# Optimization experiments

Hardware: AMD Instinct MI355X
Metric: run time of the kernel (lower is better)

Reference implementation:

```python
import jax, jax.numpy as jnp
import numpy as np

B, H, W, D = 8, 128, 128, 256
NHEAD, DK = 8, 32
WS = 8
NH, NW = H // WS, W // WS
SHIFT = WS // 2
SCALE = 1.0 / np.sqrt(DK)
WSQ = WS * WS


def _region_labels(h, w, ws, shift):
    lab = np.zeros((h, w), np.int32)
    cnt = 0
    for hs in (slice(0, h - ws), slice(h - ws, h - shift), slice(h - shift, h)):
        for vs in (slice(0, w - ws), slice(w - ws, w - shift), slice(w - shift, w)):
            lab[hs, vs] = cnt
            cnt += 1
    return np.roll(lab, (-shift, -shift), axis=(0, 1))


def _window_labels(lab, ws, nh, nw):
    return lab.reshape(nh, ws, nw, ws).transpose(0, 2, 1, 3).reshape(nh, nw, ws * ws)


# static Swin attention mask: (nh, nw, WSQ, WSQ) bool, True = masked
_lq = _window_labels(_region_labels(H, W, WS, SHIFT), WS, NH, NW)
_lk = _window_labels(_region_labels(H, W, WS, SHIFT), WS, NH, NW)
MASK = jnp.asarray(_lq[..., :, None] != _lk[..., None, :])

# static relative position index: (WSQ, WSQ) into (2*WS-1)^2 table
_coords = np.stack(np.meshgrid(np.arange(WS), np.arange(WS), indexing='ij'), -1).reshape(-1, 2)
_rel = _coords[:, None, :] - _coords[None, :, :] + (WS - 1)  # in [0, 2*WS-2]
REL_INDEX = jnp.asarray(_rel[..., 0] * (2 * WS - 1) + _rel[..., 1])


def _cyclic_shift(t, s):
    # t: (B, nhead, H, W, d)
    return jnp.roll(t, (-s, -s), axis=(2, 3))


def _partition(t):
    # (B, nhead, H, W, d) -> (B, nhead, NH, NW, WSQ, d)
    b, nh_, _, _, d = t.shape
    t = t.reshape(b, nh_, NH, WS, NW, WS, d)
    return t.transpose(0, 1, 2, 4, 3, 5, 6).reshape(b, nh_, NH, NW, WSQ, d)


def _merge(t):
    # (B, nhead, NH, NW, WSQ, d) -> (B, nhead, H, W, d)
    b, nh_, _, _, _, d = t.shape
    t = t.reshape(b, nh_, NH, NW, WS, WS, d).transpose(0, 1, 2, 4, 3, 5, 6)
    return t.reshape(b, nh_, NH * WS, NW * WS, d)


def setup_inputs() -> dict:
    key = jax.random.key(0)
    ks = jax.random.split(key, 6)
    return {
        'x': jax.random.normal(ks[0], (B, H, W, D), jnp.float32),
        'z': jax.random.normal(ks[1], (B, H, W, D), jnp.float32),
        'Wq': jax.random.normal(ks[2], (D, D), jnp.float32) * 0.02,
        'bq': jnp.zeros((D,), jnp.float32),
        'Wkv': jax.random.normal(ks[3], (D, 2 * D), jnp.float32) * 0.02,
        'bkv': jnp.zeros((2 * D,), jnp.float32),
        'Wo': jax.random.normal(ks[4], (D, D), jnp.float32) * 0.02,
        'bo': jnp.zeros((D,), jnp.float32),
        'rel_table': jax.random.normal(ks[5], ((2 * WS - 1) ** 2, NHEAD), jnp.float32) * 0.02,
    }


def reference(x, z, Wq, bq, Wkv, bkv, Wo, bo, rel_table):
    b = x.shape[0]
    q = (x @ Wq + bq).reshape(b, H, W, NHEAD, DK).transpose(0, 3, 1, 2, 4)
    kv = (z @ Wkv + bkv).reshape(b, H, W, 2, NHEAD, DK).transpose(3, 0, 4, 1, 2, 5)
    k, v = kv[0], kv[1]

    q = _partition(_cyclic_shift(q, SHIFT))
    k = _partition(_cyclic_shift(k, SHIFT))
    v = _partition(_cyclic_shift(v, SHIFT))

    # scores: (B, nhead, NH, NW, WSQ, WSQ)
    scores = jnp.einsum('bhijqd,bhijkd->bhijqk', q, k) * SCALE
    pe = rel_table[REL_INDEX]                       # (WSQ, WSQ, nhead)
    scores = scores + pe.transpose(2, 0, 1)[None, :, None, None]
    scores = jnp.where(MASK, jnp.float32(-1e9), scores)
    attn = jax.nn.softmax(scores, axis=-1)

    out = jnp.einsum('bhijqk,bhijkd->bhijqd', attn, v)
    out = _cyclic_shift(_merge(out), -SHIFT)        # (B, nhead, H, W, DK)
    out = out.transpose(0, 2, 3, 1, 4).reshape(b, H, W, D)
    return out @ Wo + bo
```

## Files before the change

### kernel.cpp

```cpp
#include <hip/hip_runtime.h>
#include <hip/hip_bf16.h>


typedef __bf16  bf16x8 __attribute__((ext_vector_type(8)));
typedef short   short8 __attribute__((ext_vector_type(8)));
typedef float   f32x4  __attribute__((ext_vector_type(4)));

#define SCALE_F 0.17677669529663687f

#define ZS   16896
#define WB   33792
#define WSZ  5120
#define LDS_TOT 74752

__device__ __forceinline__ short f2bs(float f){
    __hip_bfloat16 h = __float2bfloat16(f);
    return __builtin_bit_cast(short, h);
}
__device__ __forceinline__ short8 cvt8(float4 a, float4 b){
    short8 t;
    t[0]=f2bs(a.x); t[1]=f2bs(a.y); t[2]=f2bs(a.z); t[3]=f2bs(a.w);
    t[4]=f2bs(b.x); t[5]=f2bs(b.y); t[6]=f2bs(b.z); t[7]=f2bs(b.w);
    return t;
}
__device__ __forceinline__ int strip3(int r, int c){
    if (c == 0) return 0;
    if (c == 1) return (r < 4) ? 0 : 1;
    return (r < 4) ? 2 : 0;
}

__global__ __launch_bounds__(256) void prep_k(const float* __restrict__ Wq,
                                              const float* __restrict__ Wkv,
                                              const float* __restrict__ Wo,
                                              const float* __restrict__ rel,
                                              short* __restrict__ Wqt,
                                              short* __restrict__ Wkvt,
                                              short* __restrict__ Wot,
                                              float* __restrict__ ADD){
    int i = blockIdx.x * 256 + threadIdx.x;
    if (i < 65536){
        int n = i >> 8, k = i & 255;
        Wqt[i] = f2bs(Wq[k * 256 + n]);
    } else if (i < 196608){
        int j = i - 65536;
        int n = j >> 8, k = j & 255;
        Wkvt[j] = f2bs(Wkv[k * 512 + n]);
    } else if (i < 262144){
        int j = i - 196608;
        int n = j >> 8, k = j & 255;
        Wot[j] = f2bs(Wo[k * 256 + n]);
    } else {
        int j = i - 262144;
        int k = j & 63, q = (j >> 6) & 63, head = (j >> 12) & 7, cls = j >> 15;
        int wiC = cls / 3, wjC = cls - wiC * 3;
        int qr = q >> 3, qc = q & 7, kr = k >> 3, kc = k & 7;
        int lq = strip3(qr, wiC) * 3 + strip3(qc, wjC);
        int lk = strip3(kr, wiC) * 3 + strip3(kc, wjC);
        float pe = rel[((qr - kr + 7) * 15 + (qc - kc + 7)) * 8 + head];
        ADD[j] = (lq != lk) ? -1e9f : pe;
    }
}

__global__ __launch_bounds__(512, 2) void fused_k(
    const float* __restrict__ x, const float* __restrict__ z,
    const short* __restrict__ Wqt, const short* __restrict__ Wkvt,
    const short* __restrict__ Wot,
    const float* __restrict__ bq, const float* __restrict__ bkv,
    const float* __restrict__ bo,
    const float* __restrict__ ADD, float* __restrict__ out){
    __shared__ __align__(16) short lds[LDS_TOT];
    const int tid = threadIdx.x, w = tid >> 6, lane = tid & 63;
    const int l15 = lane & 15, g = lane >> 4;
    const int bx = blockIdx.x;
    const int wj = bx & 15, wi = (bx >> 4) & 15, b = bx >> 8;
    const int wiC = (wi > 13) ? wi - 13 : 0;
    const int wjC = (wj > 13) ? wj - 13 : 0;
    const f32x4 zero = {0.f,0.f,0.f,0.f};

#pragma unroll
    for (int i=0;i<4;++i){
        const int u = tid + i*512;
        const int p = u >> 5, c8 = u & 31;
        const int pr = ((wi << 3) + (p >> 3) + 4) & 127;
        const int pc = ((wj << 3) + (p & 7) + 4) & 127;
        const size_t gidx = ((((((size_t)b << 7) | pr) << 7) | pc) << 8) + c8*8;
        const float4* xp = reinterpret_cast<const float4*>(x + gidx);
        float4 a0 = xp[0], a1 = xp[1];
        *reinterpret_cast<short8*>(lds + p*264 + c8*8) = cvt8(a0, a1);
        const float4* zp = reinterpret_cast<const float4*>(z + gidx);
        float4 b0 = zp[0], b1 = zp[1];
        *reinterpret_cast<short8*>(lds + ZS + p*264 + c8*8) = cvt8(b0, b1);
    }
    __syncthreads();

    short* R  = lds + WB + w*WSZ;
    short* VL = lds + w*2048;
    const int c0 = w*32;

    {
        bf16x8 wf[8][2];
#pragma unroll
        for (int kt=0;kt<8;++kt)
#pragma unroll
            for (int nj=0;nj<2;++nj)
                wf[kt][nj] = *reinterpret_cast<const bf16x8*>(Wqt + (size_t)(c0 + nj*16 + l15)*256 + kt*32 + g*8);
        f32x4 acc[4][2];
#pragma unroll
        for (int mi=0;mi<4;++mi){ acc[mi][0]=zero; acc[mi][1]=zero; }
#pragma unroll
        for (int kt=0;kt<8;++kt){
            bf16x8 af[4];
#pragma unroll
            for (int mi=0;mi<4;++mi)
                af[mi] = *reinterpret_cast<const bf16x8*>(lds + (mi*16 + l15)*264 + kt*32 + g*8);
#pragma unroll
            for (int mi=0;mi<4;++mi)
#pragma unroll
                for (int nj=0;nj<2;++nj)
                    acc[mi][nj] = __builtin_amdgcn_mfma_f32_16x16x32_bf16(af[mi], wf[kt][nj], acc[mi][nj], 0,0,0);
        }
#pragma unroll
        for (int nj=0;nj<2;++nj){
            float bv = bq[c0 + nj*16 + l15];
#pragma unroll
            for (int mi=0;mi<4;++mi)
#pragma unroll
                for (int r=0;r<4;++r)
                    R[(mi*16 + g*4 + r)*40 + nj*16 + l15] = f2bs(acc[mi][nj][r] + bv);
        }
    }
    {
        bf16x8 wf[8][2];
#pragma unroll
        for (int kt=0;kt<8;++kt)
#pragma unroll
            for (int nj=0;nj<2;++nj)
                wf[kt][nj] = *reinterpret_cast<const bf16x8*>(Wkvt + (size_t)(c0 + nj*16 + l15)*256 + kt*32 + g*8);
        f32x4 acc[4][2];
#pragma unroll
        for (int mi=0;mi<4;++mi){ acc[mi][0]=zero; acc[mi][1]=zero; }
#pragma unroll
        for (int kt=0;kt<8;++kt){
            bf16x8 af[4];
#pragma unroll
            for (int mi=0;mi<4;++mi)
                af[mi] = *reinterpret_cast<const bf16x8*>(lds + ZS + (mi*16 + l15)*264 + kt*32 + g*8);
#pragma unroll
            for (int mi=0;mi<4;++mi)
#pragma unroll
                for (int nj=0;nj<2;++nj)
                    acc[mi][nj] = __builtin_amdgcn_mfma_f32_16x16x32_bf16(af[mi], wf[kt][nj], acc[mi][nj], 0,0,0);
        }
#pragma unroll
        for (int nj=0;nj<2;++nj){
            float bv = bkv[c0 + nj*16 + l15];
#pragma unroll
            for (int mi=0;mi<4;++mi)
#pragma unroll
                for (int r=0;r<4;++r)
                    R[2560 + (mi*16 + g*4 + r)*40 + nj*16 + l15] = f2bs(acc[mi][nj][r] + bv);
        }
    }
    __syncthreads();
    {
        bf16x8 wf[8][2];
#pragma unroll
        for (int kt=0;kt<8;++kt)
#pragma unroll
            for (int nj=0;nj<2;++nj)
                wf[kt][nj] = *reinterpret_cast<const bf16x8*>(Wkvt + (size_t)(256 + c0 + nj*16 + l15)*256 + kt*32 + g*8);
        f32x4 acc[4][2];
#pragma unroll
        for (int mi=0;mi<4;++mi){ acc[mi][0]=zero; acc[mi][1]=zero; }
#pragma unroll
        for (int kt=0;kt<8;++kt){
            bf16x8 af[4];
#pragma unroll
            for (int mi=0;mi<4;++mi)
                af[mi] = *reinterpret_cast<const bf16x8*>(lds + ZS + (mi*16 + l15)*264 + kt*32 + g*8);
#pragma unroll
            for (int mi=0;mi<4;++mi)
#pragma unroll
                for (int nj=0;nj<2;++nj)
                    acc[mi][nj] = __builtin_amdgcn_mfma_f32_16x16x32_bf16(af[mi], wf[kt][nj], acc[mi][nj], 0,0,0);
        }
        const int sw = (l15 & 7) << 3;
#pragma unroll
        for (int nj=0;nj<2;++nj){
            float bv = bkv[256 + c0 + nj*16 + l15];
            const int colb = (nj*16 + l15) * 64;
#pragma unroll
            for (int mi=0;mi<4;++mi)
#pragma unroll
                for (int r=0;r<4;++r)
                    VL[(colb + mi*16 + g*4 + r) ^ sw] = f2bs(acc[mi][nj][r] + bv);
        }
    }

    bf16x8 aq[4], bk[4];
#pragma unroll
    for (int mi=0;mi<4;++mi) aq[mi] = *reinterpret_cast<const bf16x8*>(R + (mi*16 + l15)*40 + g*8);
#pragma unroll
    for (int ni=0;ni<4;++ni) bk[ni] = *reinterpret_cast<const bf16x8*>(R + 2560 + (ni*16 + l15)*40 + g*8);
    f32x4 s[4][4];
#pragma unroll
    for (int mi=0;mi<4;++mi)
#pragma unroll
        for (int ni=0;ni<4;++ni)
            s[mi][ni] = __builtin_amdgcn_mfma_f32_16x16x32_bf16(aq[mi], bk[ni], zero, 0,0,0);

    const float* addb = ADD + (size_t)(((wiC*3 + wjC)*8 + w) << 12);
    float rs[4][4];
#pragma unroll
    for (int mi=0;mi<4;++mi){
        const int qbase = mi*16 + g*4;
#pragma unroll
        for (int ni=0;ni<4;++ni){
            const int k = ni*16 + l15;
#pragma unroll
            for (int r=0;r<4;++r)
                s[mi][ni][r] = fmaf(s[mi][ni][r], SCALE_F, addb[((qbase + r) << 6) + k]);
        }
#pragma unroll
        for (int r=0;r<4;++r){
            float m = fmaxf(fmaxf(s[mi][0][r], s[mi][1][r]), fmaxf(s[mi][2][r], s[mi][3][r]));
            m = fmaxf(m, __shfl_xor(m, 1));
            m = fmaxf(m, __shfl_xor(m, 2));
            m = fmaxf(m, __shfl_xor(m, 4));
            m = fmaxf(m, __shfl_xor(m, 8));
            float sum = 0.f;
#pragma unroll
            for (int ni=0;ni<4;++ni){
                float p = __expf(s[mi][ni][r] - m);
                s[mi][ni][r] = p;
                sum += p;
            }
            sum += __shfl_xor(sum, 1);
            sum += __shfl_xor(sum, 2);
            sum += __shfl_xor(sum, 4);
            sum += __shfl_xor(sum, 8);
            rs[mi][r] = 1.f / sum;
            const int q = qbase + r;
#pragma unroll
            for (int ni=0;ni<4;++ni)
                R[q*72 + ni*16 + l15] = f2bs(s[mi][ni][r]);
        }
    }

    f32x4 o[4][2];
#pragma unroll
    for (int mi=0;mi<4;++mi){ o[mi][0]=zero; o[mi][1]=zero; }
    {
        const int sw = (l15 & 7) << 3;
#pragma unroll
        for (int ks=0;ks<2;++ks){
            bf16x8 pa[4], vb[2];
#pragma unroll
            for (int mi=0;mi<4;++mi)
                pa[mi] = *reinterpret_cast<const bf16x8*>(R + (mi*16 + l15)*72 + ks*32 + g*8);
#pragma unroll
            for (int nj=0;nj<2;++nj)
                vb[nj] = *reinterpret_cast<const bf16x8*>(VL + (((nj*16 + l15)*64 + ks*32 + g*8) ^ sw));
#pragma unroll
            for (int mi=0;mi<4;++mi)
#pragma unroll
                for (int nj=0;nj<2;++nj)
                    o[mi][nj] = __builtin_amdgcn_mfma_f32_16x16x32_bf16(pa[mi], vb[nj], o[mi][nj], 0,0,0);
        }
    }

#pragma unroll
    for (int mi=0;mi<4;++mi)
#pragma unroll
        for (int nj=0;nj<2;++nj)
#pragma unroll
            for (int r=0;r<4;++r)
                R[(mi*16 + g*4 + r)*40 + nj*16 + l15] = f2bs(o[mi][nj][r] * rs[mi][r]);
    __syncthreads();

    {
        bf16x8 wf[8][2];
#pragma unroll
        for (int kt=0;kt<8;++kt)
#pragma unroll
            for (int nj=0;nj<2;++nj)
                wf[kt][nj] = *reinterpret_cast<const bf16x8*>(Wot + (size_t)(c0 + nj*16 + l15)*256 + kt*32 + g*8);
        f32x4 acc[4][2];
#pragma unroll
        for (int mi=0;mi<4;++mi){ acc[mi][0]=zero; acc[mi][1]=zero; }
#pragma unroll
        for (int kt=0;kt<8;++kt){
            const short* areg = lds + WB + kt*WSZ;
            bf16x8 af[4];
#pragma unroll
            for (int mi=0;mi<4;++mi)
                af[mi] = *reinterpret_cast<const bf16x8*>(areg + (mi*16 + l15)*40 + g*8);
#pragma unroll
            for (int mi=0;mi<4;++mi)
#pragma unroll
                for (int nj=0;nj<2;++nj)
                    acc[mi][nj] = __builtin_amdgcn_mfma_f32_16x16x32_bf16(af[mi], wf[kt][nj], acc[mi][nj], 0,0,0);
        }
#pragma unroll
        for (int nj=0;nj<2;++nj){
            const int col = c0 + nj*16 + l15;
            const float bv = bo[col];
#pragma unroll
            for (int mi=0;mi<4;++mi)
#pragma unroll
                for (int r=0;r<4;++r){
                    const int p = mi*16 + g*4 + r;
                    const int pr = ((wi << 3) + (p >> 3) + 4) & 127;
                    const int pc = ((wj << 3) + (p & 7) + 4) & 127;
                    const size_t gp = ((((size_t)b << 7) | pr) << 7) | pc;
                    out[gp * 256 + col] = acc[mi][nj][r] + bv;
                }
        }
    }
}

extern "C" void kernel_launch(void* const* d_in, const int* in_sizes, int n_in,
                              void* d_out, int out_size, void* d_ws, size_t ws_size,
                              hipStream_t stream) {
    const float* x    = (const float*)d_in[0];
    const float* z    = (const float*)d_in[1];
    const float* Wq   = (const float*)d_in[2];
    const float* bq   = (const float*)d_in[3];
    const float* Wkv  = (const float*)d_in[4];
    const float* bkv  = (const float*)d_in[5];
    const float* Wo   = (const float*)d_in[6];
    const float* bo   = (const float*)d_in[7];
    const float* rel  = (const float*)d_in[8];

    char* ws = (char*)d_ws;
    short* Wqt  = (short*)(ws);
    short* Wkvt = (short*)(ws + 131072);
    short* Wot  = (short*)(ws + 393216);
    float* ADD  = (float*)(ws + 524288);

    prep_k<<<2176, 256, 0, stream>>>(Wq, Wkv, Wo, rel, Wqt, Wkvt, Wot, ADD);
    fused_k<<<2048, 512, 0, stream>>>(x, z, Wqt, Wkvt, Wot, bq, bkv, bo, ADD, (float*)d_out);
}
```

Measured before the change: 252.1 us.

## Split each head's window rows across two waves with 1024-thread blocks

The fused kernel now launches 1024 threads per block. Each of the eight heads is handled by two waves, and each wave processes 32 of the 64 window rows in the projections, scores, softmax, PV and output projection. This doubles resident waves per CU, since LDS already limits the kernel to one block per CU, and should give more latency hiding. In exchange it adds extra block-wide barriers to protect the shared R buffer, duplicates the weight-fragment loads per wave pair, and the (1024,4) launch bound may force a tight register budget and spilling.

```diff
diff --git a/kernel.cpp b/kernel.cpp
--- a/kernel.cpp
+++ b/kernel.cpp
@@ -61,7 +61,7 @@
     }
 }
 
-__global__ __launch_bounds__(512, 2) void fused_k(
+__global__ __launch_bounds__(1024, 4) void fused_k(
     const float* __restrict__ x, const float* __restrict__ z,
     const short* __restrict__ Wqt, const short* __restrict__ Wkvt,
     const short* __restrict__ Wot,
@@ -71,6 +71,7 @@
     __shared__ __align__(16) short lds[LDS_TOT];
     const int tid = threadIdx.x, w = tid >> 6, lane = tid & 63;
     const int l15 = lane & 15, g = lane >> 4;
+    const int h = w >> 1, m = w & 1, r0 = m * 32;
     const int bx = blockIdx.x;
     const int wj = bx & 15, wi = (bx >> 4) & 15, b = bx >> 8;
     const int wiC = (wi > 13) ? wi - 13 : 0;
@@ -78,8 +79,8 @@
     const f32x4 zero = {0.f,0.f,0.f,0.f};
 
 #pragma unroll
-    for (int i=0;i<4;++i){
-        const int u = tid + i*512;
+    for (int i=0;i<2;++i){
+        const int u = tid + i*1024;
         const int p = u >> 5, c8 = u & 31;
         const int pr = ((wi << 3) + (p >> 3) + 4) & 127;
         const int pc = ((wj << 3) + (p & 7) + 4) & 127;
@@ -93,9 +94,9 @@
     }
     __syncthreads();
 
-    short* R  = lds + WB + w*WSZ;
-    short* VL = lds + w*2048;
-    const int c0 = w*32;
+    short* R  = lds + WB + h*WSZ;
+    short* VL = lds + h*2048;
+    const int c0 = h*32;
 
     {
         bf16x8 wf[8][2];
@@ -104,17 +105,17 @@
 #pragma unroll
             for (int nj=0;nj<2;++nj)
                 wf[kt][nj] = *reinterpret_cast<const bf16x8*>(Wqt + (size_t)(c0 + nj*16 + l15)*256 + kt*32 + g*8);
-        f32x4 acc[4][2];
-#pragma unroll
-        for (int mi=0;mi<4;++mi){ acc[mi][0]=zero; acc[mi][1]=zero; }
+        f32x4 acc[2][2];
+#pragma unroll
+        for (int mi=0;mi<2;++mi){ acc[mi][0]=zero; acc[mi][1]=zero; }
 #pragma unroll
         for (int kt=0;kt<8;++kt){
-            bf16x8 af[4];
-#pragma unroll
-            for (int mi=0;mi<4;++mi)
-                af[mi] = *reinterpret_cast<const bf16x8*>(lds + (mi*16 + l15)*264 + kt*32 + g*8);
-#pragma unroll
-            for (int mi=0;mi<4;++mi)
+            bf16x8 af[2];
+#pragma unroll
+            for (int mi=0;mi<2;++mi)
+                af[mi] = *reinterpret_cast<const bf16x8*>(lds + (r0 + mi*16 + l15)*264 + kt*32 + g*8);
+#pragma unroll
+            for (int mi=0;mi<2;++mi)
 #pragma unroll
                 for (int nj=0;nj<2;++nj)
                     acc[mi][nj] = __builtin_amdgcn_mfma_f32_16x16x32_bf16(af[mi], wf[kt][nj], acc[mi][nj], 0,0,0);
@@ -123,10 +124,10 @@
         for (int nj=0;nj<2;++nj){
             float bv = bq[c0 + nj*16 + l15];
 #pragma unroll
-            for (int mi=0;mi<4;++mi)
+            for (int mi=0;mi<2;++mi)
 #pragma unroll
                 for (int r=0;r<4;++r)
-                    R[(mi*16 + g*4 + r)*40 + nj*16 + l15] = f2bs(acc[mi][nj][r] + bv);
+                    R[(r0 + mi*16 + g*4 + r)*40 + nj*16 + l15] = f2bs(acc[mi][nj][r] + bv);
         }
     }
     {
@@ -136,17 +137,17 @@
 #pragma unroll
             for (int nj=0;nj<2;++nj)
                 wf[kt][nj] = *reinterpret_cast<const bf16x8*>(Wkvt + (size_t)(c0 + nj*16 + l15)*256 + kt*32 + g*8);
-        f32x4 acc[4][2];
-#pragma unroll
-        for (int mi=0;mi<4;++mi){ acc[mi][0]=zero; acc[mi][1]=zero; }
+        f32x4 acc[2][2];
+#pragma unroll
+        for (int mi=0;mi<2;++mi){ acc[mi][0]=zero; acc[mi][1]=zero; }
 #pragma unroll
         for (int kt=0;kt<8;++kt){
-            bf16x8 af[4];
-#pragma unroll
-            for (int mi=0;mi<4;++mi)
-                af[mi] = *reinterpret_cast<const bf16x8*>(lds + ZS + (mi*16 + l15)*264 + kt*32 + g*8);
-#pragma unroll
-            for (int mi=0;mi<4;++mi)
+            bf16x8 af[2];
+#pragma unroll
+            for (int mi=0;mi<2;++mi)
+                af[mi] = *reinterpret_cast<const bf16x8*>(lds + ZS + (r0 + mi*16 + l15)*264 + kt*32 + g*8);
+#pragma unroll
+            for (int mi=0;mi<2;++mi)
 #pragma unroll
                 for (int nj=0;nj<2;++nj)
                     acc[mi][nj] = __builtin_amdgcn_mfma_f32_16x16x32_bf16(af[mi], wf[kt][nj], acc[mi][nj], 0,0,0);
@@ -155,13 +156,14 @@
         for (int nj=0;nj<2;++nj){
             float bv = bkv[c0 + nj*16 + l15];
 #pragma unroll
-            for (int mi=0;mi<4;++mi)
+            for (int mi=0;mi<2;++mi)
 #pragma unroll
                 for (int r=0;r<4;++r)
-                    R[2560 + (mi*16 + g*4 + r)*40 + nj*16 + l15] = f2bs(acc[mi][nj][r] + bv);
-        }
-    }
-    __syncthreads();
+                    R[2560 + (r0 + mi*16 + g*4 + r)*40 + nj*16 + l15] = f2bs(acc[mi][nj][r] + bv);
+        }
+    }
+    __syncthreads();
+
     {
         bf16x8 wf[8][2];
 #pragma unroll
@@ -169,17 +171,17 @@
 #pragma unroll
             for (int nj=0;nj<2;++nj)
                 wf[kt][nj] = *reinterpret_cast<const bf16x8*>(Wkvt + (size_t)(256 + c0 + nj*16 + l15)*256 + kt*32 + g*8);
-        f32x4 acc[4][2];
-#pragma unroll
-        for (int mi=0;mi<4;++mi){ acc[mi][0]=zero; acc[mi][1]=zero; }
+        f32x4 acc[2][2];
+#pragma unroll
+        for (int mi=0;mi<2;++mi){ acc[mi][0]=zero; acc[mi][1]=zero; }
 #pragma unroll
         for (int kt=0;kt<8;++kt){
-            bf16x8 af[4];
-#pragma unroll
-            for (int mi=0;mi<4;++mi)
-                af[mi] = *reinterpret_cast<const bf16x8*>(lds + ZS + (mi*16 + l15)*264 + kt*32 + g*8);
-#pragma unroll
-            for (int mi=0;mi<4;++mi)
+            bf16x8 af[2];
+#pragma unroll
+            for (int mi=0;mi<2;++mi)
+                af[mi] = *reinterpret_cast<const bf16x8*>(lds + ZS + (r0 + mi*16 + l15)*264 + kt*32 + g*8);
+#pragma unroll
+            for (int mi=0;mi<2;++mi)
 #pragma unroll
                 for (int nj=0;nj<2;++nj)
                     acc[mi][nj] = __builtin_amdgcn_mfma_f32_16x16x32_bf16(af[mi], wf[kt][nj], acc[mi][nj], 0,0,0);
@@ -190,30 +192,31 @@
             float bv = bkv[256 + c0 + nj*16 + l15];
             const int colb = (nj*16 + l15) * 64;
 #pragma unroll
-            for (int mi=0;mi<4;++mi)
+            for (int mi=0;mi<2;++mi)
 #pragma unroll
                 for (int r=0;r<4;++r)
-                    VL[(colb + mi*16 + g*4 + r) ^ sw] = f2bs(acc[mi][nj][r] + bv);
-        }
-    }
-
-    bf16x8 aq[4], bk[4];
-#pragma unroll
-    for (int mi=0;mi<4;++mi) aq[mi] = *reinterpret_cast<const bf16x8*>(R + (mi*16 + l15)*40 + g*8);
+                    VL[(colb + r0 + mi*16 + g*4 + r) ^ sw] = f2bs(acc[mi][nj][r] + bv);
+        }
+    }
+
+    bf16x8 aq[2], bk[4];
+#pragma unroll
+    for (int mi=0;mi<2;++mi) aq[mi] = *reinterpret_cast<const bf16x8*>(R + (r0 + mi*16 + l15)*40 + g*8);
 #pragma unroll
     for (int ni=0;ni<4;++ni) bk[ni] = *reinterpret_cast<const bf16x8*>(R + 2560 + (ni*16 + l15)*40 + g*8);
-    f32x4 s[4][4];
-#pragma unroll
-    for (int mi=0;mi<4;++mi)
+    f32x4 s[2][4];
+#pragma unroll
+    for (int mi=0;mi<2;++mi)
 #pragma unroll
         for (int ni=0;ni<4;++ni)
             s[mi][ni] = __builtin_amdgcn_mfma_f32_16x16x32_bf16(aq[mi], bk[ni], zero, 0,0,0);
-
-    const float* addb = ADD + (size_t)(((wiC*3 + wjC)*8 + w) << 12);
-    float rs[4][4];
-#pragma unroll
-    for (int mi=0;mi<4;++mi){
-        const int qbase = mi*16 + g*4;
+    __syncthreads();
+
+    const float* addb = ADD + (size_t)(((wiC*3 + wjC)*8 + h) << 12);
+    float rs[2][4];
+#pragma unroll
+    for (int mi=0;mi<2;++mi){
+        const int qbase = r0 + mi*16 + g*4;
 #pragma unroll
         for (int ni=0;ni<4;++ni){
             const int k = ni*16 + l15;
@@ -223,15 +226,15 @@
         }
 #pragma unroll
         for (int r=0;r<4;++r){
-            float m = fmaxf(fmaxf(s[mi][0][r], s[mi][1][r]), fmaxf(s[mi][2][r], s[mi][3][r]));
-            m = fmaxf(m, __shfl_xor(m, 1));
-            m = fmaxf(m, __shfl_xor(m, 2));
-            m = fmaxf(m, __shfl_xor(m, 4));
-            m = fmaxf(m, __shfl_xor(m, 8));
+            float mx = fmaxf(fmaxf(s[mi][0][r], s[mi][1][r]), fmaxf(s[mi][2][r], s[mi][3][r]));
+            mx = fmaxf(mx, __shfl_xor(mx, 1));
+            mx = fmaxf(mx, __shfl_xor(mx, 2));
+            mx = fmaxf(mx, __shfl_xor(mx, 4));
+            mx = fmaxf(mx, __shfl_xor(mx, 8));
             float sum = 0.f;
 #pragma unroll
             for (int ni=0;ni<4;++ni){
-                float p = __expf(s[mi][ni][r] - m);
+                float p = __expf(s[mi][ni][r] - mx);
                 s[mi][ni][r] = p;
                 sum += p;
             }
@@ -247,35 +250,36 @@
         }
     }
 
-    f32x4 o[4][2];
-#pragma unroll
-    for (int mi=0;mi<4;++mi){ o[mi][0]=zero; o[mi][1]=zero; }
+    f32x4 o[2][2];
+#pragma unroll
+    for (int mi=0;mi<2;++mi){ o[mi][0]=zero; o[mi][1]=zero; }
     {
         const int sw = (l15 & 7) << 3;
 #pragma unroll
         for (int ks=0;ks<2;++ks){
-            bf16x8 pa[4], vb[2];
-#pragma unroll
-            for (int mi=0;mi<4;++mi)
-                pa[mi] = *reinterpret_cast<const bf16x8*>(R + (mi*16 + l15)*72 + ks*32 + g*8);
+            bf16x8 pa[2], vb[2];
+#pragma unroll
+            for (int mi=0;mi<2;++mi)
+                pa[mi] = *reinterpret_cast<const bf16x8*>(R + (r0 + mi*16 + l15)*72 + ks*32 + g*8);
 #pragma unroll
             for (int nj=0;nj<2;++nj)
                 vb[nj] = *reinterpret_cast<const bf16x8*>(VL + (((nj*16 + l15)*64 + ks*32 + g*8) ^ sw));
 #pragma unroll
-            for (int mi=0;mi<4;++mi)
+            for (int mi=0;mi<2;++mi)
 #pragma unroll
                 for (int nj=0;nj<2;++nj)
                     o[mi][nj] = __builtin_amdgcn_mfma_f32_16x16x32_bf16(pa[mi], vb[nj], o[mi][nj], 0,0,0);
         }
     }
-
-#pragma unroll
-    for (int mi=0;mi<4;++mi)
+    __syncthreads();
+
+#pragma unroll
+    for (int mi=0;mi<2;++mi)
 #pragma unroll
         for (int nj=0;nj<2;++nj)
 #pragma unroll
             for (int r=0;r<4;++r)
-                R[(mi*16 + g*4 + r)*40 + nj*16 + l15] = f2bs(o[mi][nj][r] * rs[mi][r]);
+                R[(r0 + mi*16 + g*4 + r)*40 + nj*16 + l15] = f2bs(o[mi][nj][r] * rs[mi][r]);
     __syncthreads();
 
     {
@@ -285,18 +289,18 @@
 #pragma unroll
             for (int nj=0;nj<2;++nj)
                 wf[kt][nj] = *reinterpret_cast<const bf16x8*>(Wot + (size_t)(c0 + nj*16 + l15)*256 + kt*32 + g*8);
-        f32x4 acc[4][2];
-#pragma unroll
-        for (int mi=0;mi<4;++mi){ acc[mi][0]=zero; acc[mi][1]=zero; }
+        f32x4 acc[2][2];
+#pragma unroll
+        for (int mi=0;mi<2;++mi){ acc[mi][0]=zero; acc[mi][1]=zero; }
 #pragma unroll
         for (int kt=0;kt<8;++kt){
             const short* areg = lds + WB + kt*WSZ;
-            bf16x8 af[4];
-#pragma unroll
-            for (int mi=0;mi<4;++mi)
-                af[mi] = *reinterpret_cast<const bf16x8*>(areg + (mi*16 + l15)*40 + g*8);
-#pragma unroll
-            for (int mi=0;mi<4;++mi)
+            bf16x8 af[2];
+#pragma unroll
+            for (int mi=0;mi<2;++mi)
+                af[mi] = *reinterpret_cast<const bf16x8*>(areg + (r0 + mi*16 + l15)*40 + g*8);
+#pragma unroll
+            for (int mi=0;mi<2;++mi)
 #pragma unroll
                 for (int nj=0;nj<2;++nj)
                     acc[mi][nj] = __builtin_amdgcn_mfma_f32_16x16x32_bf16(af[mi], wf[kt][nj], acc[mi][nj], 0,0,0);
@@ -306,10 +310,10 @@
             const int col = c0 + nj*16 + l15;
             const float bv = bo[col];
 #pragma unroll
-            for (int mi=0;mi<4;++mi)
+            for (int mi=0;mi<2;++mi)
 #pragma unroll
                 for (int r=0;r<4;++r){
-                    const int p = mi*16 + g*4 + r;
+                    const int p = r0 + mi*16 + g*4 + r;
                     const int pr = ((wi << 3) + (p >> 3) + 4) & 127;
                     const int pc = ((wj << 3) + (p & 7) + 4) & 127;
                     const size_t gp = ((((size_t)b << 7) | pr) << 7) | pc;
@@ -339,5 +343,5 @@
     float* ADD  = (float*)(ws + 524288);
 
     prep_k<<<2176, 256, 0, stream>>>(Wq, Wkv, Wo, rel, Wqt, Wkvt, Wot, ADD);
-    fused_k<<<2048, 512, 0, stream>>>(x, z, Wqt, Wkvt, Wot, bq, bkv, bo, ADD, (float*)d_out);
-}
+    fused_k<<<2048, 1024, 0, stream>>>(x, z, Wqt, Wkvt, Wot, bq, bkv, bo, ADD, (float*)d_out);
+}
```

Result: slower. 350.0 us (+38.8%).

## Split fused window-attention kernel into QKV projection and attention+output kernels

Applied to the files above, without the earlier changes.

Breaks the single fused kernel into two. The first projects Q, K and V and writes them as bf16 to global workspace. The second, with 256 threads per block and one wave handling two heads, computes attention and the output projection. Weight fragments are now loaded once per k-step instead of being preloaded into registers, and both kernels use less LDS, aiming for lower register and LDS pressure and higher occupancy. In exchange, roughly 200 MB of extra global write-then-read traffic for Q/K/V is added, plus an extra launch.

```diff
diff --git a/kernel.cpp b/kernel.cpp
--- a/kernel.cpp
+++ b/kernel.cpp
@@ -4,14 +4,10 @@
 
 typedef __bf16  bf16x8 __attribute__((ext_vector_type(8)));
 typedef short   short8 __attribute__((ext_vector_type(8)));
+typedef short   short4v __attribute__((ext_vector_type(4)));
 typedef float   f32x4  __attribute__((ext_vector_type(4)));
 
 #define SCALE_F 0.17677669529663687f
-
-#define ZS   16896
-#define WB   33792
-#define WSZ  5120
-#define LDS_TOT 74752
 
 __device__ __forceinline__ short f2bs(float f){
     __hip_bfloat16 h = __float2bfloat16(f);
@@ -61,20 +57,16 @@
     }
 }
 
-__global__ __launch_bounds__(512, 2) void fused_k(
+__global__ __launch_bounds__(512, 2) void qkv_k(
     const float* __restrict__ x, const float* __restrict__ z,
     const short* __restrict__ Wqt, const short* __restrict__ Wkvt,
-    const short* __restrict__ Wot,
     const float* __restrict__ bq, const float* __restrict__ bkv,
-    const float* __restrict__ bo,
-    const float* __restrict__ ADD, float* __restrict__ out){
-    __shared__ __align__(16) short lds[LDS_TOT];
+    short* __restrict__ Qw, short* __restrict__ Kw, short* __restrict__ Vw){
+    __shared__ __align__(16) short lds[2 * 16896];
     const int tid = threadIdx.x, w = tid >> 6, lane = tid & 63;
     const int l15 = lane & 15, g = lane >> 4;
     const int bx = blockIdx.x;
     const int wj = bx & 15, wi = (bx >> 4) & 15, b = bx >> 8;
-    const int wiC = (wi > 13) ? wi - 13 : 0;
-    const int wjC = (wj > 13) ? wj - 13 : 0;
     const f32x4 zero = {0.f,0.f,0.f,0.f};
 
 #pragma unroll
@@ -89,27 +81,23 @@
         *reinterpret_cast<short8*>(lds + p*264 + c8*8) = cvt8(a0, a1);
         const float4* zp = reinterpret_cast<const float4*>(z + gidx);
         float4 b0 = zp[0], b1 = zp[1];
-        *reinterpret_cast<short8*>(lds + ZS + p*264 + c8*8) = cvt8(b0, b1);
+        *reinterpret_cast<short8*>(lds + 16896 + p*264 + c8*8) = cvt8(b0, b1);
     }
     __syncthreads();
 
-    short* R  = lds + WB + w*WSZ;
-    short* VL = lds + w*2048;
-    const int c0 = w*32;
+    const int c0 = w * 32;
+    const size_t base = ((((size_t)b*8 + w)*16 + wi)*16 + wj) * 2048;
 
     {
-        bf16x8 wf[8][2];
-#pragma unroll
-        for (int kt=0;kt<8;++kt)
-#pragma unroll
-            for (int nj=0;nj<2;++nj)
-                wf[kt][nj] = *reinterpret_cast<const bf16x8*>(Wqt + (size_t)(c0 + nj*16 + l15)*256 + kt*32 + g*8);
         f32x4 acc[4][2];
 #pragma unroll
         for (int mi=0;mi<4;++mi){ acc[mi][0]=zero; acc[mi][1]=zero; }
 #pragma unroll
         for (int kt=0;kt<8;++kt){
-            bf16x8 af[4];
+            bf16x8 af[4], wf[2];
+#pragma unroll
+            for (int nj=0;nj<2;++nj)
+                wf[nj] = *reinterpret_cast<const bf16x8*>(Wqt + (size_t)(c0 + nj*16 + l15)*256 + kt*32 + g*8);
 #pragma unroll
             for (int mi=0;mi<4;++mi)
                 af[mi] = *reinterpret_cast<const bf16x8*>(lds + (mi*16 + l15)*264 + kt*32 + g*8);
@@ -117,7 +105,7 @@
             for (int mi=0;mi<4;++mi)
 #pragma unroll
                 for (int nj=0;nj<2;++nj)
-                    acc[mi][nj] = __builtin_amdgcn_mfma_f32_16x16x32_bf16(af[mi], wf[kt][nj], acc[mi][nj], 0,0,0);
+                    acc[mi][nj] = __builtin_amdgcn_mfma_f32_16x16x32_bf16(af[mi], wf[nj], acc[mi][nj], 0,0,0);
         }
 #pragma unroll
         for (int nj=0;nj<2;++nj){
@@ -126,30 +114,27 @@
             for (int mi=0;mi<4;++mi)
 #pragma unroll
                 for (int r=0;r<4;++r)
-                    R[(mi*16 + g*4 + r)*40 + nj*16 + l15] = f2bs(acc[mi][nj][r] + bv);
+                    Qw[base + (size_t)(mi*16 + g*4 + r)*32 + nj*16 + l15] = f2bs(acc[mi][nj][r] + bv);
         }
     }
     {
-        bf16x8 wf[8][2];
-#pragma unroll
-        for (int kt=0;kt<8;++kt)
-#pragma unroll
-            for (int nj=0;nj<2;++nj)
-                wf[kt][nj] = *reinterpret_cast<const bf16x8*>(Wkvt + (size_t)(c0 + nj*16 + l15)*256 + kt*32 + g*8);
         f32x4 acc[4][2];
 #pragma unroll
         for (int mi=0;mi<4;++mi){ acc[mi][0]=zero; acc[mi][1]=zero; }
 #pragma unroll
         for (int kt=0;kt<8;++kt){
-            bf16x8 af[4];
-#pragma unroll
-            for (int mi=0;mi<4;++mi)
-                af[mi] = *reinterpret_cast<const bf16x8*>(lds + ZS + (mi*16 + l15)*264 + kt*32 + g*8);
+            bf16x8 af[4], wf[2];
+#pragma unroll
+            for (int nj=0;nj<2;++nj)
+                wf[nj] = *reinterpret_cast<const bf16x8*>(Wkvt + (size_t)(c0 + nj*16 + l15)*256 + kt*32 + g*8);
+#pragma unroll
+            for (int mi=0;mi<4;++mi)
+                af[mi] = *reinterpret_cast<const bf16x8*>(lds + 16896 + (mi*16 + l15)*264 + kt*32 + g*8);
 #pragma unroll
             for (int mi=0;mi<4;++mi)
 #pragma unroll
                 for (int nj=0;nj<2;++nj)
-                    acc[mi][nj] = __builtin_amdgcn_mfma_f32_16x16x32_bf16(af[mi], wf[kt][nj], acc[mi][nj], 0,0,0);
+                    acc[mi][nj] = __builtin_amdgcn_mfma_f32_16x16x32_bf16(af[mi], wf[nj], acc[mi][nj], 0,0,0);
         }
 #pragma unroll
         for (int nj=0;nj<2;++nj){
@@ -158,164 +143,178 @@
             for (int mi=0;mi<4;++mi)
 #pragma unroll
                 for (int r=0;r<4;++r)
-                    R[2560 + (mi*16 + g*4 + r)*40 + nj*16 + l15] = f2bs(acc[mi][nj][r] + bv);
-        }
-    }
-    __syncthreads();
+                    Kw[base + (size_t)(mi*16 + g*4 + r)*32 + nj*16 + l15] = f2bs(acc[mi][nj][r] + bv);
+        }
+    }
     {
-        bf16x8 wf[8][2];
-#pragma unroll
-        for (int kt=0;kt<8;++kt)
-#pragma unroll
-            for (int nj=0;nj<2;++nj)
-                wf[kt][nj] = *reinterpret_cast<const bf16x8*>(Wkvt + (size_t)(256 + c0 + nj*16 + l15)*256 + kt*32 + g*8);
         f32x4 acc[4][2];
 #pragma unroll
         for (int mi=0;mi<4;++mi){ acc[mi][0]=zero; acc[mi][1]=zero; }
 #pragma unroll
         for (int kt=0;kt<8;++kt){
-            bf16x8 af[4];
-#pragma unroll
-            for (int mi=0;mi<4;++mi)
-                af[mi] = *reinterpret_cast<const bf16x8*>(lds + ZS + (mi*16 + l15)*264 + kt*32 + g*8);
+            bf16x8 af[4], wf[2];
+#pragma unroll
+            for (int nj=0;nj<2;++nj)
+                wf[nj] = *reinterpret_cast<const bf16x8*>(Wkvt + (size_t)(256 + c0 + nj*16 + l15)*256 + kt*32 + g*8);
+#pragma unroll
+            for (int mi=0;mi<4;++mi)
+                af[mi] = *reinterpret_cast<const bf16x8*>(lds + 16896 + (mi*16 + l15)*264 + kt*32 + g*8);
 #pragma unroll
             for (int mi=0;mi<4;++mi)
 #pragma unroll
                 for (int nj=0;nj<2;++nj)
-                    acc[mi][nj] = __builtin_amdgcn_mfma_f32_16x16x32_bf16(af[mi], wf[kt][nj], acc[mi][nj], 0,0,0);
-        }
-        const int sw = (l15 & 7) << 3;
+                    acc[mi][nj] = __builtin_amdgcn_mfma_f32_16x16x32_bf16(af[mi], wf[nj], acc[mi][nj], 0,0,0);
+        }
 #pragma unroll
         for (int nj=0;nj<2;++nj){
             float bv = bkv[256 + c0 + nj*16 + l15];
-            const int colb = (nj*16 + l15) * 64;
-#pragma unroll
-            for (int mi=0;mi<4;++mi)
+            const int dk = nj*16 + l15;
+#pragma unroll
+            for (int mi=0;mi<4;++mi){
+                short4v t;
+#pragma unroll
+                for (int r=0;r<4;++r) t[r] = f2bs(acc[mi][nj][r] + bv);
+                *reinterpret_cast<short4v*>(Vw + base + (size_t)dk*64 + mi*16 + g*4) = t;
+            }
+        }
+    }
+}
+
+__global__ __launch_bounds__(256, 2) void attnO_k(
+    const short* __restrict__ Qw, const short* __restrict__ Kw,
+    const short* __restrict__ Vw, const short* __restrict__ Wot,
+    const float* __restrict__ bo, const float* __restrict__ ADD,
+    float* __restrict__ out){
+    __shared__ __align__(16) short lds[4*4608 + 16896];
+    const int tid = threadIdx.x, w = tid >> 6, lane = tid & 63;
+    const int l15 = lane & 15, g = lane >> 4;
+    const int bx = blockIdx.x;
+    const int wj = bx & 15, wi = (bx >> 4) & 15, b = bx >> 8;
+    const int wiC = (wi > 13) ? wi - 13 : 0;
+    const int wjC = (wj > 13) ? wj - 13 : 0;
+    short* P   = lds + w * 4608;
+    short* att = lds + 18432;
+    const f32x4 zero = {0.f,0.f,0.f,0.f};
+
+    for (int hh = 0; hh < 2; ++hh){
+        const int h = w + hh * 4;
+        const size_t base = ((((size_t)b*8 + h)*16 + wi)*16 + wj) * 2048;
+
+        bf16x8 aq[4], bk[4];
+#pragma unroll
+        for (int mi=0;mi<4;++mi)
+            aq[mi] = *reinterpret_cast<const bf16x8*>(Qw + base + (size_t)(mi*16 + l15)*32 + g*8);
+#pragma unroll
+        for (int ni=0;ni<4;++ni)
+            bk[ni] = *reinterpret_cast<const bf16x8*>(Kw + base + (size_t)(ni*16 + l15)*32 + g*8);
+        f32x4 s[4][4];
+#pragma unroll
+        for (int mi=0;mi<4;++mi)
+#pragma unroll
+            for (int ni=0;ni<4;++ni)
+                s[mi][ni] = __builtin_amdgcn_mfma_f32_16x16x32_bf16(aq[mi], bk[ni], zero, 0,0,0);
+
+        const float* addb = ADD + (size_t)(((wiC*3 + wjC)*8 + h) << 12);
+        float rs[4][4];
+#pragma unroll
+        for (int mi=0;mi<4;++mi){
+            const int qbase = mi*16 + g*4;
+#pragma unroll
+            for (int ni=0;ni<4;++ni){
+                const int k = ni*16 + l15;
 #pragma unroll
                 for (int r=0;r<4;++r)
-                    VL[(colb + mi*16 + g*4 + r) ^ sw] = f2bs(acc[mi][nj][r] + bv);
-        }
-    }
-
-    bf16x8 aq[4], bk[4];
-#pragma unroll
-    for (int mi=0;mi<4;++mi) aq[mi] = *reinterpret_cast<const bf16x8*>(R + (mi*16 + l15)*40 + g*8);
-#pragma unroll
-    for (int ni=0;ni<4;++ni) bk[ni] = *reinterpret_cast<const bf16x8*>(R + 2560 + (ni*16 + l15)*40 + g*8);
-    f32x4 s[4][4];
-#pragma unroll
-    for (int mi=0;mi<4;++mi)
-#pragma unroll
-        for (int ni=0;ni<4;++ni)
-            s[mi][ni] = __builtin_amdgcn_mfma_f32_16x16x32_bf16(aq[mi], bk[ni], zero, 0,0,0);
-
-    const float* addb = ADD + (size_t)(((wiC*3 + wjC)*8 + w) << 12);
-    float rs[4][4];
-#pragma unroll
-    for (int mi=0;mi<4;++mi){
-        const int qbase = mi*16 + g*4;
-#pragma unroll
-        for (int ni=0;ni<4;++ni){
-            const int k = ni*16 + l15;
-#pragma unroll
-            for (int r=0;r<4;++r)
-                s[mi][ni][r] = fmaf(s[mi][ni][r], SCALE_F, addb[((qbase + r) << 6) + k]);
-        }
-#pragma unroll
-        for (int r=0;r<4;++r){
-            float m = fmaxf(fmaxf(s[mi][0][r], s[mi][1][r]), fmaxf(s[mi][2][r], s[mi][3][r]));
-            m = fmaxf(m, __shfl_xor(m, 1));
-            m = fmaxf(m, __shfl_xor(m, 2));
-            m = fmaxf(m, __shfl_xor(m, 4));
-            m = fmaxf(m, __shfl_xor(m, 8));
-            float sum = 0.f;
-#pragma unroll
-            for (int ni=0;ni<4;++ni){
-                float p = __expf(s[mi][ni][r] - m);
-                s[mi][ni][r] = p;
-                sum += p;
+                    s[mi][ni][r] = fmaf(s[mi][ni][r], SCALE_F, addb[((qbase + r) << 6) + k]);
             }
-            sum += __shfl_xor(sum, 1);
-            sum += __shfl_xor(sum, 2);
-            sum += __shfl_xor(sum, 4);
-            sum += __shfl_xor(sum, 8);
-            rs[mi][r] = 1.f / sum;
-            const int q = qbase + r;
-#pragma unroll
-            for (int ni=0;ni<4;++ni)
-                R[q*72 + ni*16 + l15] = f2bs(s[mi][ni][r]);
-        }
-    }
-
-    f32x4 o[4][2];
-#pragma unroll
-    for (int mi=0;mi<4;++mi){ o[mi][0]=zero; o[mi][1]=zero; }
-    {
-        const int sw = (l15 & 7) << 3;
+#pragma unroll
+            for (int r=0;r<4;++r){
+                float mx = fmaxf(fmaxf(s[mi][0][r], s[mi][1][r]), fmaxf(s[mi][2][r], s[mi][3][r]));
+                mx = fmaxf(mx, __shfl_xor(mx, 1));
+                mx = fmaxf(mx, __shfl_xor(mx, 2));
+                mx = fmaxf(mx, __shfl_xor(mx, 4));
+                mx = fmaxf(mx, __shfl_xor(mx, 8));
+                float sum = 0.f;
+#pragma unroll
+                for (int ni=0;ni<4;++ni){
+                    float p = __expf(s[mi][ni][r] - mx);
+                    s[mi][ni][r] = p;
+                    sum += p;
+                }
+                sum += __shfl_xor(sum, 1);
+                sum += __shfl_xor(sum, 2);
+                sum += __shfl_xor(sum, 4);
+                sum += __shfl_xor(sum, 8);
+                rs[mi][r] = 1.f / sum;
+                const int q = qbase + r;
+#pragma unroll
+                for (int ni=0;ni<4;++ni)
+                    P[q*72 + ni*16 + l15] = f2bs(s[mi][ni][r]);
+            }
+        }
+
+        f32x4 o[4][2];
+#pragma unroll
+        for (int mi=0;mi<4;++mi){ o[mi][0]=zero; o[mi][1]=zero; }
 #pragma unroll
         for (int ks=0;ks<2;++ks){
             bf16x8 pa[4], vb[2];
 #pragma unroll
             for (int mi=0;mi<4;++mi)
-                pa[mi] = *reinterpret_cast<const bf16x8*>(R + (mi*16 + l15)*72 + ks*32 + g*8);
-#pragma unroll
-            for (int nj=0;nj<2;++nj)
-                vb[nj] = *reinterpret_cast<const bf16x8*>(VL + (((nj*16 + l15)*64 + ks*32 + g*8) ^ sw));
+                pa[mi] = *reinterpret_cast<const bf16x8*>(P + (mi*16 + l15)*72 + ks*32 + g*8);
+#pragma unroll
+            for (int nj=0;nj<2;++nj)
+                vb[nj] = *reinterpret_cast<const bf16x8*>(Vw + base + (size_t)(nj*16 + l15)*64 + ks*32 + g*8);
 #pragma unroll
             for (int mi=0;mi<4;++mi)
 #pragma unroll
                 for (int nj=0;nj<2;++nj)
                     o[mi][nj] = __builtin_amdgcn_mfma_f32_16x16x32_bf16(pa[mi], vb[nj], o[mi][nj], 0,0,0);
         }
-    }
-
+
+#pragma unroll
+        for (int mi=0;mi<4;++mi)
+#pragma unroll
+            for (int nj=0;nj<2;++nj)
+#pragma unroll
+                for (int r=0;r<4;++r)
+                    att[(mi*16 + g*4 + r)*264 + h*32 + nj*16 + l15] = f2bs(o[mi][nj][r] * rs[mi][r]);
+    }
+    __syncthreads();
+
+    f32x4 acc[4][4];
 #pragma unroll
     for (int mi=0;mi<4;++mi)
 #pragma unroll
-        for (int nj=0;nj<2;++nj)
-#pragma unroll
-            for (int r=0;r<4;++r)
-                R[(mi*16 + g*4 + r)*40 + nj*16 + l15] = f2bs(o[mi][nj][r] * rs[mi][r]);
-    __syncthreads();
-
-    {
-        bf16x8 wf[8][2];
-#pragma unroll
-        for (int kt=0;kt<8;++kt)
-#pragma unroll
-            for (int nj=0;nj<2;++nj)
-                wf[kt][nj] = *reinterpret_cast<const bf16x8*>(Wot + (size_t)(c0 + nj*16 + l15)*256 + kt*32 + g*8);
-        f32x4 acc[4][2];
-#pragma unroll
-        for (int mi=0;mi<4;++mi){ acc[mi][0]=zero; acc[mi][1]=zero; }
-#pragma unroll
-        for (int kt=0;kt<8;++kt){
-            const short* areg = lds + WB + kt*WSZ;
-            bf16x8 af[4];
-#pragma unroll
-            for (int mi=0;mi<4;++mi)
-                af[mi] = *reinterpret_cast<const bf16x8*>(areg + (mi*16 + l15)*40 + g*8);
-#pragma unroll
-            for (int mi=0;mi<4;++mi)
-#pragma unroll
-                for (int nj=0;nj<2;++nj)
-                    acc[mi][nj] = __builtin_amdgcn_mfma_f32_16x16x32_bf16(af[mi], wf[kt][nj], acc[mi][nj], 0,0,0);
-        }
-#pragma unroll
-        for (int nj=0;nj<2;++nj){
-            const int col = c0 + nj*16 + l15;
-            const float bv = bo[col];
-#pragma unroll
-            for (int mi=0;mi<4;++mi)
-#pragma unroll
-                for (int r=0;r<4;++r){
-                    const int p = mi*16 + g*4 + r;
-                    const int pr = ((wi << 3) + (p >> 3) + 4) & 127;
-                    const int pc = ((wj << 3) + (p & 7) + 4) & 127;
-                    const size_t gp = ((((size_t)b << 7) | pr) << 7) | pc;
-                    out[gp * 256 + col] = acc[mi][nj][r] + bv;
-                }
-        }
+        for (int nj=0;nj<4;++nj) acc[mi][nj] = zero;
+#pragma unroll
+    for (int kt=0;kt<8;++kt){
+        bf16x8 af[4], bfm[4];
+#pragma unroll
+        for (int mi=0;mi<4;++mi)
+            af[mi] = *reinterpret_cast<const bf16x8*>(att + (mi*16 + l15)*264 + kt*32 + g*8);
+#pragma unroll
+        for (int nj=0;nj<4;++nj)
+            bfm[nj] = *reinterpret_cast<const bf16x8*>(Wot + (size_t)(w*64 + nj*16 + l15)*256 + kt*32 + g*8);
+#pragma unroll
+        for (int mi=0;mi<4;++mi)
+#pragma unroll
+            for (int nj=0;nj<4;++nj)
+                acc[mi][nj] = __builtin_amdgcn_mfma_f32_16x16x32_bf16(af[mi], bfm[nj], acc[mi][nj], 0,0,0);
+    }
+#pragma unroll
+    for (int nj=0;nj<4;++nj){
+        const int col = w*64 + nj*16 + l15;
+        const float bv = bo[col];
+#pragma unroll
+        for (int mi=0;mi<4;++mi)
+#pragma unroll
+            for (int r=0;r<4;++r){
+                const int p = mi*16 + g*4 + r;
+                const int pr = ((wi << 3) + (p >> 3) + 4) & 127;
+                const int pc = ((wj << 3) + (p & 7) + 4) & 127;
+                const size_t gp = ((((size_t)b << 7) | pr) << 7) | pc;
+                out[gp * 256 + col] = acc[mi][nj][r] + bv;
+            }
     }
 }
 
@@ -337,7 +336,11 @@
     short* Wkvt = (short*)(ws + 131072);
     short* Wot  = (short*)(ws + 393216);
     float* ADD  = (float*)(ws + 524288);
-
-    prep_k<<<2176, 256, 0, stream>>>(Wq, Wkv, Wo, rel, Wqt, Wkvt, Wot, ADD);
-    fused_k<<<2048, 512, 0, stream>>>(x, z, Wqt, Wkvt, Wot, bq, bkv, bo, ADD, (float*)d_out);
-}
+    short* Qw   = (short*)(ws + 2097152);
+    short* Kw   = (short*)(ws + 69206016);
+    short* Vw   = (short*)(ws + 136314880);
+
+    prep_k <<<2176, 256, 0, stream>>>(Wq, Wkv, Wo, rel, Wqt, Wkvt, Wot, ADD);
+    qkv_k  <<<2048, 512, 0, stream>>>(x, z, Wqt, Wkvt, bq, bkv, Qw, Kw, Vw);
+    attnO_k<<<2048, 256, 0, stream>>>(Qw, Kw, Vw, Wot, bo, ADD, (float*)d_out);
+}
```

Result: slower. 274.1 us (+8.7%).
